# Kernel tuning notes

Measured on AMD Instinct MI355X. Metric: run time of the kernel, lower is better.

The kernel has to match this reference:

```python
import jax, jax.numpy as jnp
import numpy as np

CLIP_RATIO = 1.0
MAX_QINT = 127.0   # 2**(8-1) - 1
MIN_QINT = -128.0


def setup_inputs() -> dict:
    key = jax.random.key(0)
    k1, k2, k3 = jax.random.split(key, 3)
    B, S, IN, OUT = 4, 2048, 4096, 4096
    x = jax.random.normal(k1, (B, S, IN), dtype=jnp.float32)
    # pre-quantized int8 weight (out_features, in_features)
    weight = jax.random.randint(k2, (OUT, IN), -127, 128, dtype=jnp.int32).astype(jnp.int8)
    # per-output-channel dequant scale, positive, modest magnitude
    weight_scale = (jax.random.uniform(k3, (OUT, 1), dtype=jnp.float32) * 0.01 + 1e-4)
    return {"x": x, "weight": weight, "weight_scale": weight_scale}


def reference(x, weight, weight_scale):
    # per-token symmetric abs-max quantize along last dim
    mag = jnp.max(jnp.abs(x), axis=-1, keepdims=True) * CLIP_RATIO   # [B,S,1]
    a_s = jnp.where(mag == 0, 1.0, mag / MAX_QINT)                   # activation scale
    a = jnp.clip(jnp.round(x / a_s), MIN_QINT, MAX_QINT).astype(jnp.int8)
    acc = jnp.matmul(a.astype(jnp.int32), weight.T.astype(jnp.int32))  # [B,S,OUT]
    # dequant: row activation scale * per-out-channel weight scale
    out = acc.astype(jnp.float32) * a_s * weight_scale.T[None, :, :].reshape(1, 1, -1)
    return out.astype(x.dtype)
```

## Files before the change

kernel.cpp:

```cpp
#include <hip/hip_runtime.h>
#include <hip/hip_bf16.h>

typedef int v4i __attribute__((ext_vector_type(4)));

__global__ __launch_bounds__(256) void pack_w_kernel(const int* __restrict__ w,
                                                     int* __restrict__ wq,
                                                     int n4) {
    int i = blockIdx.x * 256 + threadIdx.x;
    if (i < n4) {
        const int4 v = reinterpret_cast<const int4*>(w)[i];
        wq[i] = (v.x & 0xFF) | ((v.y & 0xFF) << 8) |
                ((v.z & 0xFF) << 16) | ((v.w & 0xFF) << 24);
    }
}

__global__ __launch_bounds__(256) void quant_row4096_kernel(
    const float* __restrict__ x, int* __restrict__ aq,
    float* __restrict__ a_s) {
    const int lane = threadIdx.x & 63;
    const int wave = threadIdx.x >> 6;
    const int row  = blockIdx.x * 4 + wave;

    const float4* xr = reinterpret_cast<const float4*>(x + (size_t)row * 4096);

    float4 v[16];
#pragma unroll
    for (int i = 0; i < 16; ++i) v[i] = xr[i * 64 + lane];

    float m = 0.f;
#pragma unroll
    for (int i = 0; i < 16; ++i)
        m = fmaxf(m, fmaxf(fmaxf(fabsf(v[i].x), fabsf(v[i].y)),
                           fmaxf(fabsf(v[i].z), fabsf(v[i].w))));
#pragma unroll
    for (int off = 32; off; off >>= 1) m = fmaxf(m, __shfl_xor(m, off));

    const float as = (m == 0.f) ? 1.f : (m / 127.0f);
    if (lane == 0) a_s[row] = as;

    int* aqr = aq + (size_t)row * 1024;
#pragma unroll
    for (int i = 0; i < 16; ++i) {
        int q0 = min(127, max(-128, (int)rintf(v[i].x / as)));
        int q1 = min(127, max(-128, (int)rintf(v[i].y / as)));
        int q2 = min(127, max(-128, (int)rintf(v[i].z / as)));
        int q3 = min(127, max(-128, (int)rintf(v[i].w / as)));
        aqr[i * 64 + lane] = (q0 & 0xFF) | ((q1 & 0xFF) << 8) |
                             ((q2 & 0xFF) << 16) | ((q3 & 0xFF) << 24);
    }
}

__global__ __launch_bounds__(256) void quant_kernel(const float* __restrict__ x,
                                                    int* __restrict__ aq,
                                                    float* __restrict__ a_s,
                                                    int K) {
    const int row = blockIdx.x;
    const float4* xr = reinterpret_cast<const float4*>(x + (size_t)row * K);
    const int K4 = K >> 2;

    float m = 0.f;
    for (int i = threadIdx.x; i < K4; i += 256) {
        float4 v = xr[i];
        m = fmaxf(m, fmaxf(fmaxf(fabsf(v.x), fabsf(v.y)),
                           fmaxf(fabsf(v.z), fabsf(v.w))));
    }
#pragma unroll
    for (int off = 32; off; off >>= 1) m = fmaxf(m, __shfl_xor(m, off));

    __shared__ float red[4];
    if ((threadIdx.x & 63) == 0) red[threadIdx.x >> 6] = m;
    __syncthreads();
    m = fmaxf(fmaxf(red[0], red[1]), fmaxf(red[2], red[3]));

    const float as = (m == 0.f) ? 1.f : (m / 127.0f);
    if (threadIdx.x == 0) a_s[row] = as;

    int* aqr = aq + (size_t)row * K4;
    for (int i = threadIdx.x; i < K4; i += 256) {
        float4 v = xr[i];
        int q0 = min(127, max(-128, (int)rintf(v.x / as)));
        int q1 = min(127, max(-128, (int)rintf(v.y / as)));
        int q2 = min(127, max(-128, (int)rintf(v.z / as)));
        int q3 = min(127, max(-128, (int)rintf(v.w / as)));
        aqr[i] = (q0 & 0xFF) | ((q1 & 0xFF) << 8) |
                 ((q2 & 0xFF) << 16) | ((q3 & 0xFF) << 24);
    }
}

__global__ __launch_bounds__(256) void gemm_i8_kernel(
    const signed char* __restrict__ Aq,
    const signed char* __restrict__ Wq,
    const float* __restrict__ a_s,
    const float* __restrict__ w_s,
    float* __restrict__ out,
    int M, int N, int K) {

    __shared__ __align__(16) signed char As[128 * 64];
    __shared__ __align__(16) signed char Bs[128 * 64];

    const int t    = threadIdx.x;
    const int lane = t & 63;
    const int wave = t >> 6;
    const int wr   = wave >> 1;
    const int wc   = wave & 1;

    const int tile_m = blockIdx.y * 128;
    const int tile_n = blockIdx.x * 128;

    v4i acc[4][4];
#pragma unroll
    for (int m = 0; m < 4; ++m)
#pragma unroll
        for (int n = 0; n < 4; ++n) acc[m][n] = (v4i){0, 0, 0, 0};

    const int srow = t >> 2;
    const int scol = (t & 3) * 16;
    const signed char* gA = Aq + (size_t)(tile_m + srow) * K + scol;
    const signed char* gB = Wq + (size_t)(tile_n + srow) * K + scol;

    signed char* lA0 = &As[t * 16];
    signed char* lA1 = &As[4096 + t * 16];
    signed char* lB0 = &Bs[t * 16];
    signed char* lB1 = &Bs[4096 + t * 16];

    const int fr = lane & 15;
    const int fq = lane >> 4;
    const int a_off = (wr * 64 + fr) * 64 + fq * 16;
    const int b_off = (wc * 64 + fr) * 64 + fq * 16;

    const size_t rowstep = (size_t)64 * K;
    const int nk = K >> 6;
    for (int kt = 0; kt < nk; ++kt) {
        __syncthreads();
        __builtin_amdgcn_global_load_lds(
            (const __attribute__((address_space(1))) void*)gA,
            (__attribute__((address_space(3))) void*)lA0, 16, 0, 0);
        __builtin_amdgcn_global_load_lds(
            (const __attribute__((address_space(1))) void*)(gA + rowstep),
            (__attribute__((address_space(3))) void*)lA1, 16, 0, 0);
        __builtin_amdgcn_global_load_lds(
            (const __attribute__((address_space(1))) void*)gB,
            (__attribute__((address_space(3))) void*)lB0, 16, 0, 0);
        __builtin_amdgcn_global_load_lds(
            (const __attribute__((address_space(1))) void*)(gB + rowstep),
            (__attribute__((address_space(3))) void*)lB1, 16, 0, 0);
        gA += 64;
        gB += 64;
        __syncthreads();

        v4i af[4], bf[4];
#pragma unroll
        for (int m = 0; m < 4; ++m)
            af[m] = *reinterpret_cast<const v4i*>(As + a_off + m * 16 * 64);
#pragma unroll
        for (int n = 0; n < 4; ++n)
            bf[n] = *reinterpret_cast<const v4i*>(Bs + b_off + n * 16 * 64);

#pragma unroll
        for (int m = 0; m < 4; ++m)
#pragma unroll
            for (int n = 0; n < 4; ++n)
                acc[m][n] = __builtin_amdgcn_mfma_i32_16x16x64_i8(
                    af[m], bf[n], acc[m][n], 0, 0, 0);
    }

#pragma unroll
    for (int n = 0; n < 4; ++n) {
        const int gcol = tile_n + wc * 64 + n * 16 + fr;
        const float ws = w_s[gcol];
#pragma unroll
        for (int m = 0; m < 4; ++m) {
            const int rbase = tile_m + wr * 64 + m * 16 + fq * 4;
#pragma unroll
            for (int j = 0; j < 4; ++j) {
                const int grow = rbase + j;
                out[(size_t)grow * N + gcol] =
                    (float)acc[m][n][j] * a_s[grow] * ws;
            }
        }
    }
}

extern "C" void kernel_launch(void* const* d_in, const int* in_sizes, int n_in,
                              void* d_out, int out_size, void* d_ws, size_t ws_size,
                              hipStream_t stream) {
    const float* x      = (const float*)d_in[0];
    const int*   w      = (const int*)d_in[1];
    const float* wscale = (const float*)d_in[2];

    const int N = in_sizes[2];
    const int K = in_sizes[1] / N;
    const int M = in_sizes[0] / K;

    signed char* aq = (signed char*)d_ws;
    signed char* wq = aq + (size_t)M * K;
    float* as_buf   = (float*)(wq + (size_t)N * K);

    const int n4 = (N * K) >> 2;
    pack_w_kernel<<<(n4 + 255) / 256, 256, 0, stream>>>(w, (int*)wq, n4);

    if (K == 4096 && (M & 3) == 0) {
        quant_row4096_kernel<<<M / 4, 256, 0, stream>>>(x, (int*)aq, as_buf);
    } else {
        quant_kernel<<<M, 256, 0, stream>>>(x, (int*)aq, as_buf, K);
    }

    dim3 grid(N / 128, M / 128);
    gemm_i8_kernel<<<grid, 256, 0, stream>>>(aq, wq, as_buf, wscale,
                                             (float*)d_out, M, N, K);
}
```

Baseline: 468.6 us.

## Add 256x256 double-buffered swizzled int8 MFMA GEMM with 8 waves

Adds a new GEMM kernel that computes 256x256 output tiles with 512 threads (8 waves). It uses a K=128 tile that is double-buffered in 128KB of LDS, loaded with global_load_lds, and XOR-swizzles the LDS layout to avoid bank conflicts. Blocks are remapped so neighbouring workgroups share tiles in cache, and s_setprio is raised around the MFMA bursts. The aim is more data reuse per loaded byte and overlap of global loads with compute, at the cost of large LDS use and only 16x32=512 workgroups on the chip.

```diff
diff --git a/kernel.cpp b/kernel.cpp
--- a/kernel.cpp
+++ b/kernel.cpp
@@ -87,7 +87,7 @@
     }
 }
 
-__global__ __launch_bounds__(256) void gemm_i8_kernel(
+__global__ __launch_bounds__(512, 2) void gemm_i8_8p(
     const signed char* __restrict__ Aq,
     const signed char* __restrict__ Wq,
     const float* __restrict__ a_s,
@@ -95,73 +95,125 @@
     float* __restrict__ out,
     int M, int N, int K) {
 
-    __shared__ __align__(16) signed char As[128 * 64];
-    __shared__ __align__(16) signed char Bs[128 * 64];
-
-    const int t    = threadIdx.x;
-    const int lane = t & 63;
-    const int wave = t >> 6;
-    const int wr   = wave >> 1;
-    const int wc   = wave & 1;
-
-    const int tile_m = blockIdx.y * 128;
-    const int tile_n = blockIdx.x * 128;
-
-    v4i acc[4][4];
-#pragma unroll
-    for (int m = 0; m < 4; ++m)
-#pragma unroll
-        for (int n = 0; n < 4; ++n) acc[m][n] = (v4i){0, 0, 0, 0};
-
-    const int srow = t >> 2;
-    const int scol = (t & 3) * 16;
-    const signed char* gA = Aq + (size_t)(tile_m + srow) * K + scol;
-    const signed char* gB = Wq + (size_t)(tile_n + srow) * K + scol;
-
-    signed char* lA0 = &As[t * 16];
-    signed char* lA1 = &As[4096 + t * 16];
-    signed char* lB0 = &Bs[t * 16];
-    signed char* lB1 = &Bs[4096 + t * 16];
-
-    const int fr = lane & 15;
-    const int fq = lane >> 4;
-    const int a_off = (wr * 64 + fr) * 64 + fq * 16;
-    const int b_off = (wc * 64 + fr) * 64 + fq * 16;
-
-    const size_t rowstep = (size_t)64 * K;
-    const int nk = K >> 6;
-    for (int kt = 0; kt < nk; ++kt) {
-        __syncthreads();
+    __shared__ __align__(16) signed char lds[131072];
+
+    const int th   = threadIdx.x;
+    const int lane = th & 63;
+    const int wave = th >> 6;
+    const int wr   = wave >> 2;
+    const int wc   = wave & 3;
+    const int fr   = lane & 15;
+    const int fq   = lane >> 4;
+    const int sw   = (fr & 7) << 4;
+
+    const int nmt = M >> 8;
+    const int nnt = N >> 8;
+    const int nwg = nmt * nnt;
+    int id = blockIdx.x;
+    if ((nwg & 7) == 0) id = (id & 7) * (nwg >> 3) + (id >> 3);
+    const int tile_n = (id / nmt) << 8;
+    const int tile_m = (id % nmt) << 8;
+
+    const int srow8 = th >> 3;
+    const int scol  = (((th & 7) ^ (srow8 & 7)) << 4);
+    const signed char* ga[4];
+    const signed char* gb[4];
+#pragma unroll
+    for (int c = 0; c < 4; ++c) {
+        ga[c] = Aq + (size_t)(tile_m + c * 64 + srow8) * K + scol;
+        gb[c] = Wq + (size_t)(tile_n + c * 64 + srow8) * K + scol;
+    }
+    const int ldst = th << 4;
+
+    v4i acc[8][4];
+#pragma unroll
+    for (int i = 0; i < 8; ++i)
+#pragma unroll
+        for (int j = 0; j < 4; ++j) acc[i][j] = (v4i){0, 0, 0, 0};
+
+    const int abase = (wr * 128 + fr) * 128 + fq * 16;
+    const int bbase = (wc * 64  + fr) * 128 + fq * 16;
+    const int nkt   = K >> 7;
+
+#pragma unroll
+    for (int c = 0; c < 4; ++c) {
         __builtin_amdgcn_global_load_lds(
-            (const __attribute__((address_space(1))) void*)gA,
-            (__attribute__((address_space(3))) void*)lA0, 16, 0, 0);
+            (const __attribute__((address_space(1))) void*)(ga[c]),
+            (__attribute__((address_space(3))) void*)&lds[c * 8192 + ldst], 16, 0, 0);
         __builtin_amdgcn_global_load_lds(
-            (const __attribute__((address_space(1))) void*)(gA + rowstep),
-            (__attribute__((address_space(3))) void*)lA1, 16, 0, 0);
-        __builtin_amdgcn_global_load_lds(
-            (const __attribute__((address_space(1))) void*)gB,
-            (__attribute__((address_space(3))) void*)lB0, 16, 0, 0);
-        __builtin_amdgcn_global_load_lds(
-            (const __attribute__((address_space(1))) void*)(gB + rowstep),
-            (__attribute__((address_space(3))) void*)lB1, 16, 0, 0);
-        gA += 64;
-        gB += 64;
-        __syncthreads();
-
-        v4i af[4], bf[4];
-#pragma unroll
-        for (int m = 0; m < 4; ++m)
-            af[m] = *reinterpret_cast<const v4i*>(As + a_off + m * 16 * 64);
-#pragma unroll
-        for (int n = 0; n < 4; ++n)
-            bf[n] = *reinterpret_cast<const v4i*>(Bs + b_off + n * 16 * 64);
-
-#pragma unroll
-        for (int m = 0; m < 4; ++m)
-#pragma unroll
-            for (int n = 0; n < 4; ++n)
-                acc[m][n] = __builtin_amdgcn_mfma_i32_16x16x64_i8(
-                    af[m], bf[n], acc[m][n], 0, 0, 0);
+            (const __attribute__((address_space(1))) void*)(gb[c]),
+            (__attribute__((address_space(3))) void*)&lds[32768 + c * 8192 + ldst], 16, 0, 0);
+    }
+    asm volatile("s_waitcnt vmcnt(0)" ::: "memory");
+    __builtin_amdgcn_s_barrier();
+
+    for (int kt = 0; kt < nkt; ++kt) {
+        const int cur = kt & 1;
+        const int cA  = cur * 65536;
+        const int cB  = cA + 32768;
+        const int nA  = (cur ^ 1) * 65536;
+
+        if (kt + 1 < nkt) {
+            const int koff = (kt + 1) << 7;
+#pragma unroll
+            for (int c = 0; c < 4; ++c) {
+                __builtin_amdgcn_global_load_lds(
+                    (const __attribute__((address_space(1))) void*)(ga[c] + koff),
+                    (__attribute__((address_space(3))) void*)&lds[nA + c * 8192 + ldst], 16, 0, 0);
+                __builtin_amdgcn_global_load_lds(
+                    (const __attribute__((address_space(1))) void*)(gb[c] + koff),
+                    (__attribute__((address_space(3))) void*)&lds[nA + 32768 + c * 8192 + ldst], 16, 0, 0);
+            }
+        }
+
+        v4i a[4][2], b[2][2];
+#pragma unroll
+        for (int mg = 0; mg < 2; ++mg) {
+#pragma unroll
+            for (int mm = 0; mm < 4; ++mm)
+#pragma unroll
+                for (int ks = 0; ks < 2; ++ks)
+                    a[mm][ks] = *reinterpret_cast<const v4i*>(
+                        &lds[cA + ((abase + (mg * 4 + mm) * 2048 + ks * 64) ^ sw)]);
+#pragma unroll
+            for (int nn = 0; nn < 2; ++nn)
+#pragma unroll
+                for (int ks = 0; ks < 2; ++ks)
+                    b[nn][ks] = *reinterpret_cast<const v4i*>(
+                        &lds[cB + ((bbase + nn * 2048 + ks * 64) ^ sw)]);
+            __builtin_amdgcn_s_barrier();
+            __builtin_amdgcn_s_setprio(1);
+#pragma unroll
+            for (int mm = 0; mm < 4; ++mm)
+#pragma unroll
+                for (int nn = 0; nn < 2; ++nn)
+#pragma unroll
+                    for (int ks = 0; ks < 2; ++ks)
+                        acc[mg * 4 + mm][nn] = __builtin_amdgcn_mfma_i32_16x16x64_i8(
+                            a[mm][ks], b[nn][ks], acc[mg * 4 + mm][nn], 0, 0, 0);
+            __builtin_amdgcn_s_setprio(0);
+            __builtin_amdgcn_s_barrier();
+#pragma unroll
+            for (int nn = 0; nn < 2; ++nn)
+#pragma unroll
+                for (int ks = 0; ks < 2; ++ks)
+                    b[nn][ks] = *reinterpret_cast<const v4i*>(
+                        &lds[cB + ((bbase + (2 + nn) * 2048 + ks * 64) ^ sw)]);
+            __builtin_amdgcn_s_barrier();
+            __builtin_amdgcn_s_setprio(1);
+#pragma unroll
+            for (int mm = 0; mm < 4; ++mm)
+#pragma unroll
+                for (int nn = 0; nn < 2; ++nn)
+#pragma unroll
+                    for (int ks = 0; ks < 2; ++ks)
+                        acc[mg * 4 + mm][2 + nn] = __builtin_amdgcn_mfma_i32_16x16x64_i8(
+                            a[mm][ks], b[nn][ks], acc[mg * 4 + mm][2 + nn], 0, 0, 0);
+            __builtin_amdgcn_s_setprio(0);
+            if (mg == 1 && kt + 1 < nkt)
+                asm volatile("s_waitcnt vmcnt(0)" ::: "memory");
+            __builtin_amdgcn_s_barrier();
+        }
     }
 
 #pragma unroll
@@ -169,8 +221,8 @@
         const int gcol = tile_n + wc * 64 + n * 16 + fr;
         const float ws = w_s[gcol];
 #pragma unroll
-        for (int m = 0; m < 4; ++m) {
-            const int rbase = tile_m + wr * 64 + m * 16 + fq * 4;
+        for (int m = 0; m < 8; ++m) {
+            const int rbase = tile_m + wr * 128 + m * 16 + fq * 4;
 #pragma unroll
             for (int j = 0; j < 4; ++j) {
                 const int grow = rbase + j;
@@ -181,6 +233,75 @@
     }
 }
 
+__global__ __launch_bounds__(256) void gemm_i8_kernel(
+    const signed char* __restrict__ Aq, const signed char* __restrict__ Wq,
+    const float* __restrict__ a_s, const float* __restrict__ w_s,
+    float* __restrict__ out, int M, int N, int K) {
+
+    __shared__ __align__(16) signed char As[128 * 64];
+    __shared__ __align__(16) signed char Bs[128 * 64];
+
+    const int t = threadIdx.x, lane = t & 63, wave = t >> 6;
+    const int wr = wave >> 1, wc = wave & 1;
+    const int tile_m = blockIdx.y * 128, tile_n = blockIdx.x * 128;
+
+    v4i acc[4][4];
+#pragma unroll
+    for (int m = 0; m < 4; ++m)
+#pragma unroll
+        for (int n = 0; n < 4; ++n) acc[m][n] = (v4i){0, 0, 0, 0};
+
+    const int srow = t >> 2, scol = (t & 3) * 16;
+    const signed char* gA = Aq + (size_t)(tile_m + srow) * K + scol;
+    const signed char* gB = Wq + (size_t)(tile_n + srow) * K + scol;
+    signed char* lA0 = &As[t * 16]; signed char* lA1 = &As[4096 + t * 16];
+    signed char* lB0 = &Bs[t * 16]; signed char* lB1 = &Bs[4096 + t * 16];
+
+    const int fr = lane & 15, fq = lane >> 4;
+    const int a_off = (wr * 64 + fr) * 64 + fq * 16;
+    const int b_off = (wc * 64 + fr) * 64 + fq * 16;
+    const size_t rowstep = (size_t)64 * K;
+    const int nk = K >> 6;
+    for (int kt = 0; kt < nk; ++kt) {
+        __syncthreads();
+        __builtin_amdgcn_global_load_lds((const __attribute__((address_space(1))) void*)gA,
+            (__attribute__((address_space(3))) void*)lA0, 16, 0, 0);
+        __builtin_amdgcn_global_load_lds((const __attribute__((address_space(1))) void*)(gA + rowstep),
+            (__attribute__((address_space(3))) void*)lA1, 16, 0, 0);
+        __builtin_amdgcn_global_load_lds((const __attribute__((address_space(1))) void*)gB,
+            (__attribute__((address_space(3))) void*)lB0, 16, 0, 0);
+        __builtin_amdgcn_global_load_lds((const __attribute__((address_space(1))) void*)(gB + rowstep),
+            (__attribute__((address_space(3))) void*)lB1, 16, 0, 0);
+        gA += 64; gB += 64;
+        __syncthreads();
+
+        v4i af[4], bf[4];
+#pragma unroll
+        for (int m = 0; m < 4; ++m)
+            af[m] = *reinterpret_cast<const v4i*>(As + a_off + m * 16 * 64);
+#pragma unroll
+        for (int n = 0; n < 4; ++n)
+            bf[n] = *reinterpret_cast<const v4i*>(Bs + b_off + n * 16 * 64);
+#pragma unroll
+        for (int m = 0; m < 4; ++m)
+#pragma unroll
+            for (int n = 0; n < 4; ++n)
+                acc[m][n] = __builtin_amdgcn_mfma_i32_16x16x64_i8(af[m], bf[n], acc[m][n], 0, 0, 0);
+    }
+#pragma unroll
+    for (int n = 0; n < 4; ++n) {
+        const int gcol = tile_n + wc * 64 + n * 16 + fr;
+        const float ws = w_s[gcol];
+#pragma unroll
+        for (int m = 0; m < 4; ++m) {
+            const int rbase = tile_m + wr * 64 + m * 16 + fq * 4;
+#pragma unroll
+            for (int j = 0; j < 4; ++j)
+                out[(size_t)(rbase + j) * N + gcol] = (float)acc[m][n][j] * a_s[rbase + j] * ws;
+        }
+    }
+}
+
 extern "C" void kernel_launch(void* const* d_in, const int* in_sizes, int n_in,
                               void* d_out, int out_size, void* d_ws, size_t ws_size,
                               hipStream_t stream) {
@@ -205,7 +326,13 @@
         quant_kernel<<<M, 256, 0, stream>>>(x, (int*)aq, as_buf, K);
     }
 
-    dim3 grid(N / 128, M / 128);
-    gemm_i8_kernel<<<grid, 256, 0, stream>>>(aq, wq, as_buf, wscale,
-                                             (float*)d_out, M, N, K);
-}
+    if ((M & 255) == 0 && (N & 255) == 0 && (K & 127) == 0) {
+        const int nwg = (M >> 8) * (N >> 8);
+        gemm_i8_8p<<<nwg, 512, 0, stream>>>(aq, wq, as_buf, wscale,
+                                            (float*)d_out, M, N, K);
+    } else {
+        dim3 grid(N / 128, M / 128);
+        gemm_i8_kernel<<<grid, 256, 0, stream>>>(aq, wq, as_buf, wscale,
+                                                 (float*)d_out, M, N, K);
+    }
+}
```

Measured after the change: 435.1 us. 1.08x faster.
